# Performance work log

Hardware: AMD Instinct MI355X
Metric: run time of the kernel (lower is better)

The kernel has to match this reference:

```python
import jax, jax.numpy as jnp
import numpy as np


def setup_inputs() -> dict:
    key = jax.random.key(0)
    k1, k2, k3 = jax.random.split(key, 3)
    B, N, Lq, Ld, D = 32, 8, 256, 512, 768
    questions = jax.random.normal(k1, (B, Lq, D), dtype=jnp.float32)
    docs = jax.random.normal(k2, (B, N, Ld, D), dtype=jnp.float32)
    is_ans = jax.random.randint(k3, (B, N), 0, 2).astype(jnp.bool_)
    return {"questions": questions, "docs": docs, "is_ans": is_ans}


def reference(questions, docs, is_ans):
    # questions: [B, Lq, D]; docs: [B, N, Ld, D]; is_ans: [B, N] bool
    q_mean = questions.mean(axis=1)        # [B, D]
    d_mean = docs.mean(axis=2)             # [B, N, D]
    sim = jnp.einsum('bd,bnd->bn', q_mean, d_mean)  # [B, N]
    # loss -= sim where is_ans else loss += sim
    sign = jnp.where(is_ans, -1.0, 1.0).astype(sim.dtype)
    loss = jnp.sum(sign * sim)
    return loss
```

## Files before the change

### kernel.cpp

```cpp
#include <hip/hip_runtime.h>

typedef float f32x4 __attribute__((ext_vector_type(4)));

#define BB 32
#define NN 8
#define LQ 256
#define LD 512
#define DD 768
#define D4 (DD / 4)

#define QCH 8
#define QROWS (LQ / QCH)
#define QPART_ELEMS (QCH * BB * DD)

#define CH 16
#define LCHUNK (LD / CH)
#define NBLK (BB * NN * CH)

__global__ void __launch_bounds__(192)
qsum_kernel(const float* __restrict__ q, float* __restrict__ qpart) {
    int b = blockIdx.x;
    int c = blockIdx.y;
    int t = threadIdx.x;

    const f32x4* p = (const f32x4*)(q + ((size_t)b * LQ + (size_t)c * QROWS) * DD) + t;

    f32x4 z = {0.f, 0.f, 0.f, 0.f};
    f32x4 acc[8];
#pragma unroll
    for (int i = 0; i < 8; ++i) acc[i] = z;

#pragma unroll
    for (int i = 0; i < QROWS; ++i)
        acc[i & 7] += __builtin_nontemporal_load(p + (size_t)i * D4);

    f32x4 r = ((acc[0] + acc[1]) + (acc[2] + acc[3])) +
              ((acc[4] + acc[5]) + (acc[6] + acc[7]));
    ((f32x4*)qpart)[((size_t)c * BB + b) * D4 + t] = r;
}

__global__ void __launch_bounds__(192)
docs_kernel(const float* __restrict__ docs, const int* __restrict__ is_ans,
            const float* __restrict__ qpart, float* __restrict__ partials) {
    int bn    = blockIdx.x / CH;
    int chunk = blockIdx.x - bn * CH;
    int b     = bn >> 3;
    int t     = threadIdx.x;

    f32x4 qv = {0.f, 0.f, 0.f, 0.f};
#pragma unroll
    for (int c = 0; c < QCH; ++c)
        qv += ((const f32x4*)qpart)[((size_t)c * BB + b) * D4 + t];

    const f32x4* p = (const f32x4*)(docs + ((size_t)bn * LD + (size_t)chunk * LCHUNK) * DD) + t;

    f32x4 z = {0.f, 0.f, 0.f, 0.f};
    f32x4 acc[8];
#pragma unroll
    for (int i = 0; i < 8; ++i) acc[i] = z;

#pragma unroll
    for (int l0 = 0; l0 < LCHUNK; l0 += 8) {
        f32x4 v[8];
#pragma unroll
        for (int k = 0; k < 8; ++k)
            v[k] = __builtin_nontemporal_load(p + (size_t)(l0 + k) * D4);
#pragma unroll
        for (int k = 0; k < 8; ++k)
            acc[k] += v[k] * qv;
    }

    f32x4 r = ((acc[0] + acc[1]) + (acc[2] + acc[3])) +
              ((acc[4] + acc[5]) + (acc[6] + acc[7]));
    float s = r.x + r.y + r.z + r.w;

    for (int off = 32; off > 0; off >>= 1)
        s += __shfl_down(s, off, 64);

    __shared__ float wsum[3];
    if ((t & 63) == 0) wsum[t >> 6] = s;
    __syncthreads();
    if (t == 0) {
        float sign = is_ans[bn] ? -1.f : 1.f;
        partials[blockIdx.x] = (wsum[0] + wsum[1] + wsum[2]) * sign;
    }
}

__global__ void __launch_bounds__(256)
finish_kernel(const float* __restrict__ partials, float* __restrict__ out) {
    int t = threadIdx.x;
    float s = 0.f;
#pragma unroll
    for (int i = 0; i < NBLK; i += 256)
        s += partials[i + t];
    for (int off = 32; off > 0; off >>= 1)
        s += __shfl_down(s, off, 64);
    __shared__ float wsum[4];
    if ((t & 63) == 0) wsum[t >> 6] = s;
    __syncthreads();
    if (t == 0)
        out[0] = (wsum[0] + wsum[1] + wsum[2] + wsum[3]) * (1.f / ((float)LQ * (float)LD));
}

extern "C" void kernel_launch(void* const* d_in, const int* in_sizes, int n_in,
                              void* d_out, int out_size, void* d_ws, size_t ws_size,
                              hipStream_t stream) {
    const float* q      = (const float*)d_in[0];
    const float* docs   = (const float*)d_in[1];
    const int*   is_ans = (const int*)d_in[2];
    float* out = (float*)d_out;

    float* qpart    = (float*)d_ws;
    float* partials = qpart + QPART_ELEMS;

    qsum_kernel<<<dim3(BB, QCH), 192, 0, stream>>>(q, qpart);
    docs_kernel<<<dim3(NBLK), 192, 0, stream>>>(docs, is_ans, qpart, partials);
    finish_kernel<<<1, 256, 0, stream>>>(partials, out);
}
```

Before: 502.7 us.

## Fuse three kernels into one cooperative kernel with grid syncs

Merges the question-sum, docs dot-product and final reduction kernels into a single cooperative launch separated by grid-wide syncs. This cuts the number of launches and the gaps between kernels. It also shrinks the docs grid from 16 to 4 chunks per (b,n) pair, giving 1024 blocks so all of them can be co-resident. Nontemporal loads become plain loads and the loops are only partially unrolled. The cost is grid-sync overhead, lower parallelism with longer per-block streams, and a single phase-1 stage that stalls on the qsum blocks.

```diff
diff --git a/kernel.cpp b/kernel.cpp
--- a/kernel.cpp
+++ b/kernel.cpp
@@ -1,4 +1,7 @@
 #include <hip/hip_runtime.h>
+#include <hip/hip_cooperative_groups.h>
+
+namespace cg = cooperative_groups;
 
 typedef float f32x4 __attribute__((ext_vector_type(4)));
 
@@ -13,93 +16,96 @@
 #define QROWS (LQ / QCH)
 #define QPART_ELEMS (QCH * BB * DD)
 
-#define CH 16
+#define CH 4
 #define LCHUNK (LD / CH)
 #define NBLK (BB * NN * CH)
 
-__global__ void __launch_bounds__(192)
-qsum_kernel(const float* __restrict__ q, float* __restrict__ qpart) {
-    int b = blockIdx.x;
-    int c = blockIdx.y;
-    int t = threadIdx.x;
+__global__ void __launch_bounds__(192, 4)
+fused_kernel(const float* __restrict__ q, const float* __restrict__ docs,
+             const int* __restrict__ is_ans, float* __restrict__ qpart,
+             float* __restrict__ partials, float* __restrict__ out) {
+    cg::grid_group grid = cg::this_grid();
+    const int blk = blockIdx.x;
+    const int t   = threadIdx.x;
+    __shared__ float wsum[3];
 
-    const f32x4* p = (const f32x4*)(q + ((size_t)b * LQ + (size_t)c * QROWS) * DD) + t;
-
-    f32x4 z = {0.f, 0.f, 0.f, 0.f};
-    f32x4 acc[8];
+    if (blk < BB * QCH) {
+        int b = blk >> 3;
+        int c = blk & 7;
+        const f32x4* p = (const f32x4*)(q + ((size_t)b * LQ + (size_t)c * QROWS) * DD) + t;
+        f32x4 z = {0.f, 0.f, 0.f, 0.f};
+        f32x4 acc[8];
 #pragma unroll
-    for (int i = 0; i < 8; ++i) acc[i] = z;
-
+        for (int i = 0; i < 8; ++i) acc[i] = z;
+#pragma unroll 2
+        for (int i0 = 0; i0 < QROWS; i0 += 8) {
+            f32x4 v[8];
 #pragma unroll
-    for (int i = 0; i < QROWS; ++i)
-        acc[i & 7] += __builtin_nontemporal_load(p + (size_t)i * D4);
-
-    f32x4 r = ((acc[0] + acc[1]) + (acc[2] + acc[3])) +
-              ((acc[4] + acc[5]) + (acc[6] + acc[7]));
-    ((f32x4*)qpart)[((size_t)c * BB + b) * D4 + t] = r;
-}
-
-__global__ void __launch_bounds__(192)
-docs_kernel(const float* __restrict__ docs, const int* __restrict__ is_ans,
-            const float* __restrict__ qpart, float* __restrict__ partials) {
-    int bn    = blockIdx.x / CH;
-    int chunk = blockIdx.x - bn * CH;
-    int b     = bn >> 3;
-    int t     = threadIdx.x;
-
-    f32x4 qv = {0.f, 0.f, 0.f, 0.f};
+            for (int k = 0; k < 8; ++k) v[k] = p[(size_t)(i0 + k) * D4];
 #pragma unroll
-    for (int c = 0; c < QCH; ++c)
-        qv += ((const f32x4*)qpart)[((size_t)c * BB + b) * D4 + t];
-
-    const f32x4* p = (const f32x4*)(docs + ((size_t)bn * LD + (size_t)chunk * LCHUNK) * DD) + t;
-
-    f32x4 z = {0.f, 0.f, 0.f, 0.f};
-    f32x4 acc[8];
-#pragma unroll
-    for (int i = 0; i < 8; ++i) acc[i] = z;
-
-#pragma unroll
-    for (int l0 = 0; l0 < LCHUNK; l0 += 8) {
-        f32x4 v[8];
-#pragma unroll
-        for (int k = 0; k < 8; ++k)
-            v[k] = __builtin_nontemporal_load(p + (size_t)(l0 + k) * D4);
-#pragma unroll
-        for (int k = 0; k < 8; ++k)
-            acc[k] += v[k] * qv;
+            for (int k = 0; k < 8; ++k) acc[k] += v[k];
+        }
+        f32x4 r = ((acc[0] + acc[1]) + (acc[2] + acc[3])) +
+                  ((acc[4] + acc[5]) + (acc[6] + acc[7]));
+        ((f32x4*)qpart)[((size_t)c * BB + b) * D4 + t] = r;
     }
 
-    f32x4 r = ((acc[0] + acc[1]) + (acc[2] + acc[3])) +
-              ((acc[4] + acc[5]) + (acc[6] + acc[7]));
-    float s = r.x + r.y + r.z + r.w;
+    grid.sync();
 
-    for (int off = 32; off > 0; off >>= 1)
-        s += __shfl_down(s, off, 64);
+    {
+        int bn    = blk >> 2;
+        int chunk = blk & 3;
+        int b     = bn >> 3;
 
-    __shared__ float wsum[3];
-    if ((t & 63) == 0) wsum[t >> 6] = s;
-    __syncthreads();
-    if (t == 0) {
-        float sign = is_ans[bn] ? -1.f : 1.f;
-        partials[blockIdx.x] = (wsum[0] + wsum[1] + wsum[2]) * sign;
+        f32x4 qv = {0.f, 0.f, 0.f, 0.f};
+#pragma unroll
+        for (int c = 0; c < QCH; ++c)
+            qv += ((const f32x4*)qpart)[((size_t)c * BB + b) * D4 + t];
+
+        const f32x4* p = (const f32x4*)(docs + ((size_t)bn * LD + (size_t)chunk * LCHUNK) * DD) + t;
+
+        f32x4 z = {0.f, 0.f, 0.f, 0.f};
+        f32x4 acc[8];
+#pragma unroll
+        for (int i = 0; i < 8; ++i) acc[i] = z;
+
+#pragma unroll 2
+        for (int l0 = 0; l0 < LCHUNK; l0 += 8) {
+            f32x4 v[8];
+#pragma unroll
+            for (int k = 0; k < 8; ++k) v[k] = p[(size_t)(l0 + k) * D4];
+#pragma unroll
+            for (int k = 0; k < 8; ++k) acc[k] += v[k] * qv;
+        }
+
+        f32x4 r = ((acc[0] + acc[1]) + (acc[2] + acc[3])) +
+                  ((acc[4] + acc[5]) + (acc[6] + acc[7]));
+        float s = r.x + r.y + r.z + r.w;
+
+        for (int off = 32; off > 0; off >>= 1)
+            s += __shfl_down(s, off, 64);
+
+        if ((t & 63) == 0) wsum[t >> 6] = s;
+        __syncthreads();
+        if (t == 0) {
+            float sign = is_ans[bn] ? -1.f : 1.f;
+            partials[blk] = (wsum[0] + wsum[1] + wsum[2]) * sign;
+        }
     }
-}
 
-__global__ void __launch_bounds__(256)
-finish_kernel(const float* __restrict__ partials, float* __restrict__ out) {
-    int t = threadIdx.x;
-    float s = 0.f;
-#pragma unroll
-    for (int i = 0; i < NBLK; i += 256)
-        s += partials[i + t];
-    for (int off = 32; off > 0; off >>= 1)
-        s += __shfl_down(s, off, 64);
-    __shared__ float wsum[4];
-    if ((t & 63) == 0) wsum[t >> 6] = s;
-    __syncthreads();
-    if (t == 0)
-        out[0] = (wsum[0] + wsum[1] + wsum[2] + wsum[3]) * (1.f / ((float)LQ * (float)LD));
+    grid.sync();
+
+    if (blk == 0) {
+        float s = 0.f;
+        for (int i = t; i < NBLK; i += 192)
+            s += partials[i];
+        for (int off = 32; off > 0; off >>= 1)
+            s += __shfl_down(s, off, 64);
+        if ((t & 63) == 0) wsum[t >> 6] = s;
+        __syncthreads();
+        if (t == 0)
+            out[0] = (wsum[0] + wsum[1] + wsum[2]) * (1.f / ((float)LQ * (float)LD));
+    }
 }
 
 extern "C" void kernel_launch(void* const* d_in, const int* in_sizes, int n_in,
@@ -113,7 +119,8 @@
     float* qpart    = (float*)d_ws;
     float* partials = qpart + QPART_ELEMS;
 
-    qsum_kernel<<<dim3(BB, QCH), 192, 0, stream>>>(q, qpart);
-    docs_kernel<<<dim3(NBLK), 192, 0, stream>>>(docs, is_ans, qpart, partials);
-    finish_kernel<<<1, 256, 0, stream>>>(partials, out);
+    void* args[] = { (void*)&q, (void*)&docs, (void*)&is_ans,
+                     (void*)&qpart, (void*)&partials, (void*)&out };
+    hipLaunchCooperativeKernel(reinterpret_cast<void*>(&fused_kernel),
+                               dim3(NBLK), dim3(192), args, 0, stream);
 }
```

Result: slower. 741.5 us (+47.5%).
